# Optimization experiments

Hardware: AMD Instinct MI355X
Metric: run time of the kernel (lower is better)

The kernel has to match this reference:

```python
import jax, jax.numpy as jnp
import numpy as np
from jax import lax

LAMBD = 1.0
KAPPA = 0.1
N_ITERS = 400  # fixed unroll count; PGD converges well within this for these scales


def _project_simplex(v):
    # Euclidean projection of each row of v onto {w : w >= 0, sum(w) = 1}.
    n = v.shape[-1]
    u = -jnp.sort(-v, axis=-1)                       # descending sort
    css = jnp.cumsum(u, axis=-1)
    j = jnp.arange(1, n + 1, dtype=v.dtype)
    cond = u + (1.0 - css) / j > 0                   # monotone condition; rho = #True
    rho = jnp.sum(cond, axis=-1, keepdims=True)      # [B,1], always >= 1
    css_rho = jnp.take_along_axis(css, rho - 1, axis=-1)
    tau = (css_rho - 1.0) / rho.astype(v.dtype)
    return jnp.maximum(v - tau, 0.0)


def _solve_robust_mvo(mu, U, A):
    # min_w -mu'w + kappa*||A w||_2 + (lambd/2)*||U w||_2^2  s.t. w in simplex
    B, n = mu.shape
    G1 = jnp.einsum('bij,bik->bjk', U, U)            # U^T U, [B,n,n]
    G2 = jnp.einsum('bij,bik->bjk', A, A)            # A^T A, [B,n,n]
    # Lipschitz upper bound via Frobenius norms -> safe fixed step size
    froU2 = jnp.sum(U * U, axis=(-2, -1), keepdims=False)[:, None]   # ||U||_F^2, [B,1]
    froA = jnp.sqrt(jnp.sum(A * A, axis=(-2, -1)))[:, None]          # ||A||_F,   [B,1]
    step = 1.0 / (LAMBD * froU2 + KAPPA * froA + 1.0)

    w0 = jnp.full((B, n), 1.0 / n, dtype=mu.dtype)

    def body(w, _):
        g1w = jnp.einsum('bij,bj->bi', G1, w)        # U^T U w
        g2w = jnp.einsum('bij,bj->bi', G2, w)        # A^T A w
        nrm = jnp.sqrt(jnp.maximum(jnp.sum(w * g2w, axis=-1, keepdims=True), 1e-12))
        grad = -mu + LAMBD * g1w + KAPPA * g2w / nrm
        w_new = _project_simplex(w - step * grad)
        return w_new, None

    w, _ = lax.scan(body, w0, None, length=N_ITERS)
    # mirror the torch post-processing: clamp + renormalize
    w = jnp.maximum(w, 0.0)
    return w / (jnp.sum(w, axis=-1, keepdims=True) + 1e-12)


def setup_inputs() -> dict:
    key = jax.random.key(0)
    k1, k2, k3 = jax.random.split(key, 3)
    B, n = 512, 256
    mu = jax.random.normal(k1, (B, n), dtype=jnp.float32)
    U = jax.random.normal(k2, (B, n, n), dtype=jnp.float32)
    A = jax.random.normal(k3, (B, n, n), dtype=jnp.float32)
    return {"mu": mu, "U": U, "A": A}


def reference(mu, U, A):
    return _solve_robust_mvo(mu, U, A)
```

## Files before the change

kernel.cpp:

```cpp
#include <hip/hip_runtime.h>
#include <math.h>

#define NB 512
#define NN 256
#define N_ITERS 400
#define KAPPA_F 0.1f

typedef _Float16 half2_t __attribute__((ext_vector_type(2)));
typedef _Float16 half8_t __attribute__((ext_vector_type(8)));

__device__ inline float fdot2f(half2_t a, half2_t b, float c) {
#if __has_builtin(__builtin_amdgcn_fdot2)
  return __builtin_amdgcn_fdot2(a, b, c, false);
#else
  return (float)a.x * (float)b.x + (float)a.y * (float)b.y + c;
#endif
}


#define PAIR(V, K) __builtin_shufflevector(V, V, 2*(K), 2*(K)+1)

#define DOT8(ACC, R, UH) \
  ACC = fdot2f(PAIR(R,0), PAIR(UH,0), ACC); \
  ACC = fdot2f(PAIR(R,1), PAIR(UH,1), ACC); \
  ACC = fdot2f(PAIR(R,2), PAIR(UH,2), ACC); \
  ACC = fdot2f(PAIR(R,3), PAIR(UH,3), ACC);

#define ZC(P,J) c##P##J.x=0.f; c##P##J.y=0.f; c##P##J.z=0.f; c##P##J.w=0.f;
#define ZALL() ZC(A,0) ZC(A,1) ZC(A,2) ZC(A,3) ZC(A,4) ZC(A,5) ZC(A,6) ZC(A,7) \
               ZC(B,0) ZC(B,1) ZC(B,2) ZC(B,3) ZC(B,4) ZC(B,5) ZC(B,6) ZC(B,7)

#define GMA(J,F) { cA##J.x=fmaf(a0,F.x,cA##J.x); cA##J.y=fmaf(a0,F.y,cA##J.y); \
                   cA##J.z=fmaf(a0,F.z,cA##J.z); cA##J.w=fmaf(a0,F.w,cA##J.w); }
#define GMB(J,F) { cB##J.x=fmaf(a1,F.x,cB##J.x); cB##J.y=fmaf(a1,F.y,cB##J.y); \
                   cB##J.z=fmaf(a1,F.z,cB##J.z); cB##J.w=fmaf(a1,F.w,cB##J.w); }

#define GRAM2(SRC, RB, DOFRO) do { \
  const float4* __restrict__ src4 = (const float4*)(SRC); \
  ZALL() \
  float4 st0 = src4[t], st1 = src4[512 + t]; \
  _Pragma("unroll 1") \
  for (int kt = 0; kt < 16; ++kt) { \
    __syncthreads(); \
    ((float4*)As)[t] = st0; \
    ((float4*)As)[512 + t] = st1; \
    if (DOFRO) { fro += st0.x*st0.x + st0.y*st0.y + st0.z*st0.z + st0.w*st0.w; \
                 fro += st1.x*st1.x + st1.y*st1.y + st1.z*st1.z + st1.w*st1.w; } \
    __syncthreads(); \
    if (kt < 15) { st0 = src4[(kt+1)*1024 + t]; st1 = src4[(kt+1)*1024 + 512 + t]; } \
    _Pragma("unroll 1") \
    for (int k = 0; k < 16; ++k) { \
      const float* rowp = As + k * NN; \
      float a0 = rowp[(RB) + lane]; \
      float a1 = rowp[(RB) + 64 + lane]; \
      const float4* rp4 = (const float4*)(rowp + 32 * wv); \
      { float4 f0=rp4[0], f1=rp4[1], f2=rp4[2], f3=rp4[3]; \
        GMA(0,f0) GMA(1,f1) GMA(2,f2) GMA(3,f3) \
        GMB(0,f0) GMB(1,f1) GMB(2,f2) GMB(3,f3) } \
      { float4 f4=rp4[4], f5=rp4[5], f6=rp4[6], f7=rp4[7]; \
        GMA(4,f4) GMA(5,f5) GMA(6,f6) GMA(7,f7) \
        GMB(4,f4) GMB(5,f5) GMB(6,f6) GMB(7,f7) } \
    } \
  } \
} while (0)

#define PACK8(RREG, M, DIAG, FA, FB) { \
  float x0=FA.x, x1=FA.y, x2=FA.z, x3=FA.w; \
  float x4=FB.x, x5=FB.y, x6=FB.z, x7=FB.w; \
  const int cb = 32*wv + 8*(M); \
  if (cb+0==row_) { DIAG[row_]=x0; x0=0.f; } \
  if (cb+1==row_) { DIAG[row_]=x1; x1=0.f; } \
  if (cb+2==row_) { DIAG[row_]=x2; x2=0.f; } \
  if (cb+3==row_) { DIAG[row_]=x3; x3=0.f; } \
  if (cb+4==row_) { DIAG[row_]=x4; x4=0.f; } \
  if (cb+5==row_) { DIAG[row_]=x5; x5=0.f; } \
  if (cb+6==row_) { DIAG[row_]=x6; x6=0.f; } \
  if (cb+7==row_) { DIAG[row_]=x7; x7=0.f; } \
  half8_t h8; \
  h8[0]=(_Float16)x0; h8[1]=(_Float16)x1; h8[2]=(_Float16)x2; h8[3]=(_Float16)x3; \
  h8[4]=(_Float16)x4; h8[5]=(_Float16)x5; h8[6]=(_Float16)x6; h8[7]=(_Float16)x7; \
  RREG = h8; }

#define PACKG(PFX, CP, DIAG, RB) { const int row_ = (RB) + lane; \
  PACK8(PFX##0, 0, DIAG, c##CP##0, c##CP##1) \
  PACK8(PFX##1, 1, DIAG, c##CP##2, c##CP##3) \
  PACK8(PFX##2, 2, DIAG, c##CP##4, c##CP##5) \
  PACK8(PFX##3, 3, DIAG, c##CP##6, c##CP##7) }

#define COMB(I) { \
  const int rr = 64 * (I) + lane; \
  float2 x0 = parts[rr],          x1 = parts[NN + rr]; \
  float2 x2 = parts[2*NN + rr],   x3 = parts[3*NN + rr]; \
  float2 x4 = parts[4*NN + rr],   x5 = parts[5*NN + rr]; \
  float2 x6 = parts[6*NN + rr],   x7 = parts[7*NN + rr]; \
  q1##I = ((x0.x+x1.x)+(x2.x+x3.x))+((x4.x+x5.x)+(x6.x+x7.x)); \
  q2##I = ((x0.y+x1.y)+(x2.y+x3.y))+((x4.y+x5.y)+(x6.y+x7.y)); }

__global__
__attribute__((amdgpu_flat_work_group_size(512, 512)))
__attribute__((amdgpu_waves_per_eu(2, 2)))
void mvo_kernel(const float* __restrict__ mu,
                const float* __restrict__ U,
                const float* __restrict__ A,
                float* __restrict__ out)
{
  __shared__ alignas(16) float2 parts[8 * NN];
  __shared__ alignas(16) float    wsf[NN];
  __shared__ alignas(16) _Float16 whs[NN];
  __shared__ float mus[NN];
  __shared__ float diag1[NN];
  __shared__ float diag2[NN];
  __shared__ float dslot[8];
  __shared__ float slotA[8];
  __shared__ float slotB[8];
  __shared__ int   doneflag;

  float* As = (float*)parts;

  const int t    = threadIdx.x;
  const int b    = blockIdx.x;
  const int lane = t & 63;
  const int wv   = t >> 6;

  const float* __restrict__ Ub = U + (size_t)b * NN * NN;
  const float* __restrict__ Ab = A + (size_t)b * NN * NN;

  if (t == 0) doneflag = 0;
  if (t < NN) mus[t] = mu[b * NN + t];

  half8_t eA0,eA1,eA2,eA3, eB0,eB1,eB2,eB3, eC0,eC1,eC2,eC3, eD0,eD1,eD2,eD3;
  half8_t hA0,hA1,hA2,hA3, hB0,hB1,hB2,hB3, hC0,hC1,hC2,hC3, hD0,hD1,hD2,hD3;
  float4 cA0,cA1,cA2,cA3,cA4,cA5,cA6,cA7;
  float4 cB0,cB1,cB2,cB3,cB4,cB5,cB6,cB7;
  float fro, d1, d2;

  fro = 0.f;
  GRAM2(Ab, 0, 1);
  PACKG(hA, A, diag2, 0) PACKG(hB, B, diag2, 64)
  GRAM2(Ab, 128, 0);
  PACKG(hC, A, diag2, 128) PACKG(hD, B, diag2, 192)
  d2 = fro;
  fro = 0.f;
  GRAM2(Ub, 0, 1);
  PACKG(eA, A, diag1, 0) PACKG(eB, B, diag1, 64)
  GRAM2(Ub, 128, 0);
  PACKG(eC, A, diag1, 128) PACKG(eD, B, diag1, 192)
  d1 = fro;

  #pragma unroll
  for (int m = 1; m < 64; m <<= 1) {
    d1 += __shfl_xor(d1, m, 64);
    d2 += __shfl_xor(d2, m, 64);
  }
  if (lane == 0) { slotA[wv] = d1; slotB[wv] = d2; }
  if (t < NN) { wsf[t] = 1.0f / 256.0f; whs[t] = (_Float16)(1.0f / 256.0f); }
  __syncthreads();
  float froU2 = 0.f, froA2 = 0.f;
  #pragma unroll
  for (int k = 0; k < 8; ++k) { froU2 += slotA[k]; froA2 += slotB[k]; }
  const float step = 1.0f / (froU2 + KAPPA_F * sqrtf(froA2) + 1.0f);

  const half8_t* whp = (const half8_t*)whs + 4 * wv;
  const int dsel = lane >> 5;

  #pragma unroll 1
  for (int it = 0; it < N_ITERS; ++it) {
    half8_t uh0 = whp[0], uh1 = whp[1], uh2 = whp[2], uh3 = whp[3];
    float p10=0.f, p11=0.f, p12=0.f, p13=0.f;
    float p20=0.f, p21=0.f, p22=0.f, p23=0.f;
    DOT8(p10, eA0, uh0) DOT8(p10, eA1, uh1) DOT8(p10, eA2, uh2) DOT8(p10, eA3, uh3)
    DOT8(p11, eB0, uh0) DOT8(p11, eB1, uh1) DOT8(p11, eB2, uh2) DOT8(p11, eB3, uh3)
    DOT8(p12, eC0, uh0) DOT8(p12, eC1, uh1) DOT8(p12, eC2, uh2) DOT8(p12, eC3, uh3)
    DOT8(p13, eD0, uh0) DOT8(p13, eD1, uh1) DOT8(p13, eD2, uh2) DOT8(p13, eD3, uh3)
    DOT8(p20, hA0, uh0) DOT8(p20, hA1, uh1) DOT8(p20, hA2, uh2) DOT8(p20, hA3, uh3)
    DOT8(p21, hB0, uh0) DOT8(p21, hB1, uh1) DOT8(p21, hB2, uh2) DOT8(p21, hB3, uh3)
    DOT8(p22, hC0, uh0) DOT8(p22, hC1, uh1) DOT8(p22, hC2, uh2) DOT8(p22, hC3, uh3)
    DOT8(p23, hD0, uh0) DOT8(p23, hD1, uh1) DOT8(p23, hD2, uh2) DOT8(p23, hD3, uh3)

    float w_r0 = wsf[lane],       w_r1 = wsf[64 + lane];
    float w_r2 = wsf[128 + lane], w_r3 = wsf[192 + lane];
    if (wv == dsel)     { p10 = fmaf(diag1[lane],     w_r0, p10);
                          p20 = fmaf(diag2[lane],     w_r0, p20); }
    if (wv == 2 + dsel) { p11 = fmaf(diag1[64+lane],  w_r1, p11);
                          p21 = fmaf(diag2[64+lane],  w_r1, p21); }
    if (wv == 4 + dsel) { p12 = fmaf(diag1[128+lane], w_r2, p12);
                          p22 = fmaf(diag2[128+lane], w_r2, p22); }
    if (wv == 6 + dsel) { p13 = fmaf(diag1[192+lane], w_r3, p13);
                          p23 = fmaf(diag2[192+lane], w_r3, p23); }
    float dpart = fmaf(p20, w_r0, fmaf(p21, w_r1, fmaf(p22, w_r2, p23 * w_r3)));
    #pragma unroll
    for (int m = 1; m < 64; m <<= 1) dpart += __shfl_xor(dpart, m, 64);
    parts[wv * NN + lane]       = make_float2(p10, p20);
    parts[wv * NN + 64 + lane]  = make_float2(p11, p21);
    parts[wv * NN + 128 + lane] = make_float2(p12, p22);
    parts[wv * NN + 192 + lane] = make_float2(p13, p23);
    if (lane == 0) dslot[wv] = dpart;
    __syncthreads();

    if (wv == 0) {
      float q10, q11, q12, q13, q20, q21, q22, q23;
      COMB(0) COMB(1) COMB(2) COMB(3)
      float dot = ((dslot[0]+dslot[1])+(dslot[2]+dslot[3]))
                + ((dslot[4]+dslot[5])+(dslot[6]+dslot[7]));
      float nrm = sqrtf(fmaxf(dot, 1e-12f));
      float kon = KAPPA_F / nrm;
      float v0 = w_r0 - step * (q10 + kon * q20 - mus[lane]);
      float v1 = w_r1 - step * (q11 + kon * q21 - mus[64 + lane]);
      float v2 = w_r2 - step * (q12 + kon * q22 - mus[128 + lane]);
      float v3 = w_r3 - step * (q13 + kon * q23 - mus[192 + lane]);
      float s = v0 + v1 + v2 + v3;
      #pragma unroll
      for (int m = 1; m < 64; m <<= 1) s += __shfl_xor(s, m, 64);
      float tau = (s - 1.0f) * (1.0f / 256.0f);
      float cprev = 256.0f;
      for (int ms = 0; ms < 24; ++ms) {
        float s2 = (v0 > tau ? v0 : 0.f) + (v1 > tau ? v1 : 0.f)
                 + (v2 > tau ? v2 : 0.f) + (v3 > tau ? v3 : 0.f);
        float c2 = (v0 > tau ? 1.f : 0.f) + (v1 > tau ? 1.f : 0.f)
                 + (v2 > tau ? 1.f : 0.f) + (v3 > tau ? 1.f : 0.f);
        #pragma unroll
        for (int m = 1; m < 64; m <<= 1) {
          s2 += __shfl_xor(s2, m, 64);
          c2 += __shfl_xor(c2, m, 64);
        }
        if (c2 == cprev) break;
        tau = (s2 - 1.0f) / c2;
        cprev = c2;
      }
      float nw0 = fmaxf(v0 - tau, 0.f);
      float nw1 = fmaxf(v1 - tau, 0.f);
      float nw2 = fmaxf(v2 - tau, 0.f);
      float nw3 = fmaxf(v3 - tau, 0.f);
      int same = (nw0 == w_r0) && (nw1 == w_r1) && (nw2 == w_r2) && (nw3 == w_r3);
      int conv = __all(same);
      wsf[lane]       = nw0; wsf[64 + lane]  = nw1;
      wsf[128 + lane] = nw2; wsf[192 + lane] = nw3;
      whs[lane]       = (_Float16)nw0; whs[64 + lane]  = (_Float16)nw1;
      whs[128 + lane] = (_Float16)nw2; whs[192 + lane] = (_Float16)nw3;
      if (lane == 0) doneflag = conv;
    }
    __syncthreads();
    if (doneflag) break;
  }

  if (wv == 0) {
    float w_0 = wsf[lane],       w_1 = wsf[64 + lane];
    float w_2 = wsf[128 + lane], w_3 = wsf[192 + lane];
    float s = w_0 + w_1 + w_2 + w_3;
    #pragma unroll
    for (int m = 1; m < 64; m <<= 1) s += __shfl_xor(s, m, 64);
    float inv = 1.0f / (s + 1e-12f);
    float* ob = out + b * NN;
    ob[lane]        = w_0 * inv;
    ob[64 + lane]   = w_1 * inv;
    ob[128 + lane]  = w_2 * inv;
    ob[192 + lane]  = w_3 * inv;
  }
}

extern "C" void kernel_launch(void* const* d_in, const int* in_sizes, int n_in,
                              void* d_out, int out_size, void* d_ws, size_t ws_size,
                              hipStream_t stream) {
  const float* mu = (const float*)d_in[0];
  const float* U  = (const float*)d_in[1];
  const float* A  = (const float*)d_in[2];
  float* out = (float*)d_out;
  hipLaunchKernelGGL(mvo_kernel, dim3(NB), dim3(512), 0, stream, mu, U, A, out);
}
```

Before: 2.419 ms.

## Use DPP wave reductions, warm-start simplex tau, split U Gram, relax waves_per_eu

Replaces the shuffle-xor butterfly reductions with DPP row operations for the low strides, keeping shuffles only for strides 16 and 32. The simplex projection now starts its fixed-point iteration from the previous iteration's tau, stored in shared memory, instead of from the mean. The U Gram matrix is built one 64-row block at a time to reduce live accumulator registers, and the packed fp16 matrices are stored as half2 scalars. The occupancy hint is relaxed from 2 to 1-2 waves per EU, which gives the compiler more registers but may cost latency hiding, and the one-block-at-a-time Gram build re-streams U four times.

```diff
diff --git a/kernel.cpp b/kernel.cpp
--- a/kernel.cpp
+++ b/kernel.cpp
@@ -20,16 +20,36 @@
 
 #define PAIR(V, K) __builtin_shufflevector(V, V, 2*(K), 2*(K)+1)
 
-#define DOT8(ACC, R, UH) \
-  ACC = fdot2f(PAIR(R,0), PAIR(UH,0), ACC); \
-  ACC = fdot2f(PAIR(R,1), PAIR(UH,1), ACC); \
-  ACC = fdot2f(PAIR(R,2), PAIR(UH,2), ACC); \
-  ACC = fdot2f(PAIR(R,3), PAIR(UH,3), ACC);
-
-#define ZC(P,J) c##P##J.x=0.f; c##P##J.y=0.f; c##P##J.z=0.f; c##P##J.w=0.f;
-#define ZALL() ZC(A,0) ZC(A,1) ZC(A,2) ZC(A,3) ZC(A,4) ZC(A,5) ZC(A,6) ZC(A,7) \
-               ZC(B,0) ZC(B,1) ZC(B,2) ZC(B,3) ZC(B,4) ZC(B,5) ZC(B,6) ZC(B,7)
-
+template <int CTRL>
+__device__ inline float dpp_addt(float v) {
+  int s = __builtin_amdgcn_update_dpp(0, __float_as_int(v), CTRL, 0xF, 0xF, true);
+  return v + __int_as_float(s);
+}
+__device__ inline float wave_sum(float v) {
+  v = dpp_addt<0xB1>(v);
+  v = dpp_addt<0x4E>(v);
+  v = dpp_addt<0x141>(v);
+  v = dpp_addt<0x140>(v);
+  v += __shfl_xor(v, 16, 64);
+  v += __shfl_xor(v, 32, 64);
+  return v;
+}
+__device__ inline void wave_sum2(float& a, float& b) {
+  a = dpp_addt<0xB1>(a);  b = dpp_addt<0xB1>(b);
+  a = dpp_addt<0x4E>(a);  b = dpp_addt<0x4E>(b);
+  a = dpp_addt<0x141>(a); b = dpp_addt<0x141>(b);
+  a = dpp_addt<0x140>(a); b = dpp_addt<0x140>(b);
+  a += __shfl_xor(a, 16, 64); b += __shfl_xor(b, 16, 64);
+  a += __shfl_xor(a, 32, 64); b += __shfl_xor(b, 32, 64);
+}
+
+#define DECLROW(P) half2_t P##0,P##1,P##2,P##3,P##4,P##5,P##6,P##7, \
+                           P##8,P##9,P##10,P##11,P##12,P##13,P##14,P##15;
+
+#define ZA(J) cA##J.x=0.f; cA##J.y=0.f; cA##J.z=0.f; cA##J.w=0.f;
+#define ZB(J) cB##J.x=0.f; cB##J.y=0.f; cB##J.z=0.f; cB##J.w=0.f;
+#define ZALL() ZA(0) ZA(1) ZA(2) ZA(3) ZA(4) ZA(5) ZA(6) ZA(7) \
+               ZB(0) ZB(1) ZB(2) ZB(3) ZB(4) ZB(5) ZB(6) ZB(7)
 #define GMA(J,F) { cA##J.x=fmaf(a0,F.x,cA##J.x); cA##J.y=fmaf(a0,F.y,cA##J.y); \
                    cA##J.z=fmaf(a0,F.z,cA##J.z); cA##J.w=fmaf(a0,F.w,cA##J.w); }
 #define GMB(J,F) { cB##J.x=fmaf(a1,F.x,cB##J.x); cB##J.y=fmaf(a1,F.y,cB##J.y); \
@@ -64,28 +84,67 @@
   } \
 } while (0)
 
-#define PACK8(RREG, M, DIAG, FA, FB) { \
-  float x0=FA.x, x1=FA.y, x2=FA.z, x3=FA.w; \
-  float x4=FB.x, x5=FB.y, x6=FB.z, x7=FB.w; \
-  const int cb = 32*wv + 8*(M); \
+#define GRAM1(SRC, RB, DOFRO) do { \
+  const float4* __restrict__ src4 = (const float4*)(SRC); \
+  ZA(0) ZA(1) ZA(2) ZA(3) ZA(4) ZA(5) ZA(6) ZA(7) \
+  float4 st = src4[t]; \
+  _Pragma("unroll 1") \
+  for (int kt = 0; kt < 32; ++kt) { \
+    __syncthreads(); \
+    ((float4*)As)[t] = st; \
+    if (DOFRO) fro += st.x*st.x + st.y*st.y + st.z*st.z + st.w*st.w; \
+    __syncthreads(); \
+    if (kt < 31) st = src4[(kt + 1) * 512 + t]; \
+    _Pragma("unroll 1") \
+    for (int k = 0; k < 8; ++k) { \
+      const float* rowp = As + k * NN; \
+      float a0 = rowp[(RB) + lane]; \
+      const float4* rp4 = (const float4*)(rowp + 32 * wv); \
+      { float4 f0=rp4[0], f1=rp4[1], f2=rp4[2], f3=rp4[3]; \
+        GMA(0,f0) GMA(1,f1) GMA(2,f2) GMA(3,f3) } \
+      { float4 f4=rp4[4], f5=rp4[5], f6=rp4[6], f7=rp4[7]; \
+        GMA(4,f4) GMA(5,f5) GMA(6,f6) GMA(7,f7) } \
+    } \
+  } \
+} while (0)
+
+#define PACK4(PA, PB, C, J4, DIAG) { \
+  float x0=C.x, x1=C.y, x2=C.z, x3=C.w; \
+  const int cb = 32*wv + 4*(J4); \
   if (cb+0==row_) { DIAG[row_]=x0; x0=0.f; } \
   if (cb+1==row_) { DIAG[row_]=x1; x1=0.f; } \
   if (cb+2==row_) { DIAG[row_]=x2; x2=0.f; } \
   if (cb+3==row_) { DIAG[row_]=x3; x3=0.f; } \
-  if (cb+4==row_) { DIAG[row_]=x4; x4=0.f; } \
-  if (cb+5==row_) { DIAG[row_]=x5; x5=0.f; } \
-  if (cb+6==row_) { DIAG[row_]=x6; x6=0.f; } \
-  if (cb+7==row_) { DIAG[row_]=x7; x7=0.f; } \
-  half8_t h8; \
-  h8[0]=(_Float16)x0; h8[1]=(_Float16)x1; h8[2]=(_Float16)x2; h8[3]=(_Float16)x3; \
-  h8[4]=(_Float16)x4; h8[5]=(_Float16)x5; h8[6]=(_Float16)x6; h8[7]=(_Float16)x7; \
-  RREG = h8; }
-
-#define PACKG(PFX, CP, DIAG, RB) { const int row_ = (RB) + lane; \
-  PACK8(PFX##0, 0, DIAG, c##CP##0, c##CP##1) \
-  PACK8(PFX##1, 1, DIAG, c##CP##2, c##CP##3) \
-  PACK8(PFX##2, 2, DIAG, c##CP##4, c##CP##5) \
-  PACK8(PFX##3, 3, DIAG, c##CP##6, c##CP##7) }
+  PA.x=(_Float16)x0; PA.y=(_Float16)x1; \
+  PB.x=(_Float16)x2; PB.y=(_Float16)x3; }
+
+#define PACKROW(P, CP, DIAG) { \
+  PACK4(P##0,  P##1,  c##CP##0, 0, DIAG) \
+  PACK4(P##2,  P##3,  c##CP##1, 1, DIAG) \
+  PACK4(P##4,  P##5,  c##CP##2, 2, DIAG) \
+  PACK4(P##6,  P##7,  c##CP##3, 3, DIAG) \
+  PACK4(P##8,  P##9,  c##CP##4, 4, DIAG) \
+  PACK4(P##10, P##11, c##CP##5, 5, DIAG) \
+  PACK4(P##12, P##13, c##CP##6, 6, DIAG) \
+  PACK4(P##14, P##15, c##CP##7, 7, DIAG) }
+
+#define DOTROW(ACC, P) \
+  ACC = fdot2f(P##0,  PAIR(uh0,0), ACC); \
+  ACC = fdot2f(P##1,  PAIR(uh0,1), ACC); \
+  ACC = fdot2f(P##2,  PAIR(uh0,2), ACC); \
+  ACC = fdot2f(P##3,  PAIR(uh0,3), ACC); \
+  ACC = fdot2f(P##4,  PAIR(uh1,0), ACC); \
+  ACC = fdot2f(P##5,  PAIR(uh1,1), ACC); \
+  ACC = fdot2f(P##6,  PAIR(uh1,2), ACC); \
+  ACC = fdot2f(P##7,  PAIR(uh1,3), ACC); \
+  ACC = fdot2f(P##8,  PAIR(uh2,0), ACC); \
+  ACC = fdot2f(P##9,  PAIR(uh2,1), ACC); \
+  ACC = fdot2f(P##10, PAIR(uh2,2), ACC); \
+  ACC = fdot2f(P##11, PAIR(uh2,3), ACC); \
+  ACC = fdot2f(P##12, PAIR(uh3,0), ACC); \
+  ACC = fdot2f(P##13, PAIR(uh3,1), ACC); \
+  ACC = fdot2f(P##14, PAIR(uh3,2), ACC); \
+  ACC = fdot2f(P##15, PAIR(uh3,3), ACC);
 
 #define COMB(I) { \
   const int rr = 64 * (I) + lane; \
@@ -98,7 +157,7 @@
 
 __global__
 __attribute__((amdgpu_flat_work_group_size(512, 512)))
-__attribute__((amdgpu_waves_per_eu(2, 2)))
+__attribute__((amdgpu_waves_per_eu(1, 2)))
 void mvo_kernel(const float* __restrict__ mu,
                 const float* __restrict__ U,
                 const float* __restrict__ A,
@@ -113,6 +172,7 @@
   __shared__ float dslot[8];
   __shared__ float slotA[8];
   __shared__ float slotB[8];
+  __shared__ float taus;
   __shared__ int   doneflag;
 
   float* As = (float*)parts;
@@ -125,26 +185,32 @@
   const float* __restrict__ Ub = U + (size_t)b * NN * NN;
   const float* __restrict__ Ab = A + (size_t)b * NN * NN;
 
-  if (t == 0) doneflag = 0;
+  if (t == 0) { doneflag = 0; taus = -1e30f; }
   if (t < NN) mus[t] = mu[b * NN + t];
 
-  half8_t eA0,eA1,eA2,eA3, eB0,eB1,eB2,eB3, eC0,eC1,eC2,eC3, eD0,eD1,eD2,eD3;
-  half8_t hA0,hA1,hA2,hA3, hB0,hB1,hB2,hB3, hC0,hC1,hC2,hC3, hD0,hD1,hD2,hD3;
+  DECLROW(e0_) DECLROW(e1_) DECLROW(e2_) DECLROW(e3_)
+  DECLROW(h0_) DECLROW(h1_) DECLROW(h2_) DECLROW(h3_)
   float4 cA0,cA1,cA2,cA3,cA4,cA5,cA6,cA7;
   float4 cB0,cB1,cB2,cB3,cB4,cB5,cB6,cB7;
   float fro, d1, d2;
 
   fro = 0.f;
   GRAM2(Ab, 0, 1);
-  PACKG(hA, A, diag2, 0) PACKG(hB, B, diag2, 64)
+  { const int row_ = lane;        PACKROW(h0_, A, diag2) }
+  { const int row_ = 64 + lane;   PACKROW(h1_, B, diag2) }
   GRAM2(Ab, 128, 0);
-  PACKG(hC, A, diag2, 128) PACKG(hD, B, diag2, 192)
+  { const int row_ = 128 + lane;  PACKROW(h2_, A, diag2) }
+  { const int row_ = 192 + lane;  PACKROW(h3_, B, diag2) }
   d2 = fro;
   fro = 0.f;
-  GRAM2(Ub, 0, 1);
-  PACKG(eA, A, diag1, 0) PACKG(eB, B, diag1, 64)
-  GRAM2(Ub, 128, 0);
-  PACKG(eC, A, diag1, 128) PACKG(eD, B, diag1, 192)
+  GRAM1(Ub, 0, 1);
+  { const int row_ = lane;        PACKROW(e0_, A, diag1) }
+  GRAM1(Ub, 64, 0);
+  { const int row_ = 64 + lane;   PACKROW(e1_, A, diag1) }
+  GRAM1(Ub, 128, 0);
+  { const int row_ = 128 + lane;  PACKROW(e2_, A, diag1) }
+  GRAM1(Ub, 192, 0);
+  { const int row_ = 192 + lane;  PACKROW(e3_, A, diag1) }
   d1 = fro;
 
   #pragma unroll
@@ -168,14 +234,8 @@
     half8_t uh0 = whp[0], uh1 = whp[1], uh2 = whp[2], uh3 = whp[3];
     float p10=0.f, p11=0.f, p12=0.f, p13=0.f;
     float p20=0.f, p21=0.f, p22=0.f, p23=0.f;
-    DOT8(p10, eA0, uh0) DOT8(p10, eA1, uh1) DOT8(p10, eA2, uh2) DOT8(p10, eA3, uh3)
-    DOT8(p11, eB0, uh0) DOT8(p11, eB1, uh1) DOT8(p11, eB2, uh2) DOT8(p11, eB3, uh3)
-    DOT8(p12, eC0, uh0) DOT8(p12, eC1, uh1) DOT8(p12, eC2, uh2) DOT8(p12, eC3, uh3)
-    DOT8(p13, eD0, uh0) DOT8(p13, eD1, uh1) DOT8(p13, eD2, uh2) DOT8(p13, eD3, uh3)
-    DOT8(p20, hA0, uh0) DOT8(p20, hA1, uh1) DOT8(p20, hA2, uh2) DOT8(p20, hA3, uh3)
-    DOT8(p21, hB0, uh0) DOT8(p21, hB1, uh1) DOT8(p21, hB2, uh2) DOT8(p21, hB3, uh3)
-    DOT8(p22, hC0, uh0) DOT8(p22, hC1, uh1) DOT8(p22, hC2, uh2) DOT8(p22, hC3, uh3)
-    DOT8(p23, hD0, uh0) DOT8(p23, hD1, uh1) DOT8(p23, hD2, uh2) DOT8(p23, hD3, uh3)
+    DOTROW(p10, e0_) DOTROW(p11, e1_) DOTROW(p12, e2_) DOTROW(p13, e3_)
+    DOTROW(p20, h0_) DOTROW(p21, h1_) DOTROW(p22, h2_) DOTROW(p23, h3_)
 
     float w_r0 = wsf[lane],       w_r1 = wsf[64 + lane];
     float w_r2 = wsf[128 + lane], w_r3 = wsf[192 + lane];
@@ -188,8 +248,7 @@
     if (wv == 6 + dsel) { p13 = fmaf(diag1[192+lane], w_r3, p13);
                           p23 = fmaf(diag2[192+lane], w_r3, p23); }
     float dpart = fmaf(p20, w_r0, fmaf(p21, w_r1, fmaf(p22, w_r2, p23 * w_r3)));
-    #pragma unroll
-    for (int m = 1; m < 64; m <<= 1) dpart += __shfl_xor(dpart, m, 64);
+    dpart = wave_sum(dpart);
     parts[wv * NN + lane]       = make_float2(p10, p20);
     parts[wv * NN + 64 + lane]  = make_float2(p11, p21);
     parts[wv * NN + 128 + lane] = make_float2(p12, p22);
@@ -208,21 +267,15 @@
       float v1 = w_r1 - step * (q11 + kon * q21 - mus[64 + lane]);
       float v2 = w_r2 - step * (q12 + kon * q22 - mus[128 + lane]);
       float v3 = w_r3 - step * (q13 + kon * q23 - mus[192 + lane]);
-      float s = v0 + v1 + v2 + v3;
-      #pragma unroll
-      for (int m = 1; m < 64; m <<= 1) s += __shfl_xor(s, m, 64);
-      float tau = (s - 1.0f) * (1.0f / 256.0f);
-      float cprev = 256.0f;
+      float tau = taus;
+      float cprev = -1.f;
+      #pragma unroll 1
       for (int ms = 0; ms < 24; ++ms) {
         float s2 = (v0 > tau ? v0 : 0.f) + (v1 > tau ? v1 : 0.f)
                  + (v2 > tau ? v2 : 0.f) + (v3 > tau ? v3 : 0.f);
         float c2 = (v0 > tau ? 1.f : 0.f) + (v1 > tau ? 1.f : 0.f)
                  + (v2 > tau ? 1.f : 0.f) + (v3 > tau ? 1.f : 0.f);
-        #pragma unroll
-        for (int m = 1; m < 64; m <<= 1) {
-          s2 += __shfl_xor(s2, m, 64);
-          c2 += __shfl_xor(c2, m, 64);
-        }
+        wave_sum2(s2, c2);
         if (c2 == cprev) break;
         tau = (s2 - 1.0f) / c2;
         cprev = c2;
@@ -237,7 +290,7 @@
       wsf[128 + lane] = nw2; wsf[192 + lane] = nw3;
       whs[lane]       = (_Float16)nw0; whs[64 + lane]  = (_Float16)nw1;
       whs[128 + lane] = (_Float16)nw2; whs[192 + lane] = (_Float16)nw3;
-      if (lane == 0) doneflag = conv;
+      if (lane == 0) { taus = tau; doneflag = conv; }
     }
     __syncthreads();
     if (doneflag) break;
@@ -246,9 +299,7 @@
   if (wv == 0) {
     float w_0 = wsf[lane],       w_1 = wsf[64 + lane];
     float w_2 = wsf[128 + lane], w_3 = wsf[192 + lane];
-    float s = w_0 + w_1 + w_2 + w_3;
-    #pragma unroll
-    for (int m = 1; m < 64; m <<= 1) s += __shfl_xor(s, m, 64);
+    float s = wave_sum(w_0 + w_1 + w_2 + w_3);
     float inv = 1.0f / (s + 1e-12f);
     float* ob = out + b * NN;
     ob[lane]        = w_0 * inv;
```

Result: faster. 2.133 ms (-11.8%).
